# Performance work log

Hardware: AMD Instinct MI355X
Metric: run time of the kernel (lower is better)

Reference implementation:

```python
import jax, jax.numpy as jnp
import numpy as np

EMBED_DIM = 256
HEADS = 8
HEAD_DIM = EMBED_DIM // HEADS
T = 8            # time grid points
N0, N1 = 32, 32  # spatial grid
MAX_PATCH = 16   # static slot budget per cell (last slot = grid latent token)
NEG = -1e30


def construct_grid():
    g0 = jnp.linspace(0.0, 1.0, N0)
    g1 = jnp.linspace(0.0, 1.0, N1)
    G0, G1 = jnp.meshgrid(g0, g1, indexing='ij')
    return jnp.stack([G0, G1], axis=-1)  # [N0, N1, 2]


def setup_inputs() -> dict:
    key = jax.random.key(0)
    ks = jax.random.split(key, 8)
    m, n = 4, 16384
    x = jax.random.uniform(ks[0], (m, n, 3))                       # coords: (time, s0, s1) in [0,1]
    z = jax.random.normal(ks[1], (m, n, EMBED_DIM))
    time_grid = jnp.tile(jnp.linspace(0.0, 1.0, T)[None], (m, 1))  # [m, T] uniform time grid
    latents = jax.random.normal(ks[2], (N0, N1, EMBED_DIM))
    grid = construct_grid()
    s = 1.0 / np.sqrt(EMBED_DIM)
    Wq = jax.random.normal(ks[3], (EMBED_DIM, EMBED_DIM)) * s
    Wk = jax.random.normal(ks[4], (EMBED_DIM, EMBED_DIM)) * s
    Wv = jax.random.normal(ks[5], (EMBED_DIM, EMBED_DIM)) * s
    Wo = jax.random.normal(ks[6], (EMBED_DIM, EMBED_DIM)) * s
    return {'x': x, 'z': z, 'time_grid': time_grid, 'latents': latents,
            'grid': grid, 'Wq': Wq, 'Wk': Wk, 'Wv': Wv, 'Wo': Wo}


def _cumcount(idx):
    # idx: [n] int; returns per-element count of prior occurrences of the same value
    n = idx.shape[0]
    order = jnp.argsort(idx)                 # stable
    srt = idx[order]
    ar = jnp.arange(n)
    is_start = jnp.concatenate([jnp.array([True]), srt[1:] != srt[:-1]])
    seg_start = jax.lax.cummax(jnp.where(is_start, ar, 0), axis=0)
    cc = ar - seg_start
    return jnp.zeros_like(idx).at[order].set(cc.astype(idx.dtype))


def _forward(x, z, time_grid, latents, grid, Wq, Wk, Wv, Wo):
    m, n, _ = x.shape
    t = time_grid.shape[1]
    S = t * N0 * N1
    # --- build x_grid: repeat spatial grid over (m,t), insert time coord at dim 0 ---
    xg_sp = jnp.broadcast_to(grid[None, None], (m, t, N0, N1, 2))
    tg = jnp.broadcast_to(time_grid[:, :, None, None, None], (m, t, N0, N1, 1))
    x_grid = jnp.concatenate([tg, xg_sp], axis=-1)          # [m,t,N0,N1,3]
    # --- nearest gridded neighbour (k=1): per-dim rounding on the regular grid ---
    grid_shape = jnp.array([t, N0, N1], jnp.float32)
    xg_flat = x_grid.reshape(m, S, 3)
    xmin = xg_flat.min(axis=1)                               # [m,3]
    xmax = xg_flat.max(axis=1)
    spacing = (xmax - xmin) / (grid_shape - 1.0)             # [m,3]
    multi = jnp.floor((x - xmin[:, None] + spacing[:, None] / 2) / spacing[:, None])
    multi = jnp.clip(multi, 0.0, grid_shape - 1.0)
    strides = jnp.array([N0 * N1, N1, 1], jnp.float32)
    nearest = jnp.sum(multi * strides, axis=-1).astype(jnp.int32)  # [m,n] flat cell id
    # --- per-cell slot allocation via cumulative count ---
    cum = jax.vmap(_cumcount)(nearest)                       # [m,n]
    P = MAX_PATCH
    valid = cum < (P - 1)                                    # last slot reserved for grid token
    bidx = jnp.arange(m)[:, None]
    cell = jnp.where(valid, nearest, S)                      # out-of-bounds -> dropped
    slot = jnp.minimum(cum, P - 2)
    # --- scatter points into the joint grid [m, S, P, E]; slot P-1 = grid latent ---
    joint = jnp.zeros((m, S, P, EMBED_DIM), z.dtype)
    joint = joint.at[bidx, cell, slot].set(z, mode='drop')
    z_grid_flat = jnp.broadcast_to(
        latents.reshape(1, 1, N0 * N1, EMBED_DIM), (m, t, N0 * N1, EMBED_DIM)
    ).reshape(m, S, EMBED_DIM)
    joint = joint.at[:, :, P - 1].set(z_grid_flat)
    counts = jnp.zeros((m, S), jnp.int32).at[bidx, cell].add(1, mode='drop')
    counts = jnp.minimum(counts, P - 1)
    att_mask = jnp.concatenate(
        [jnp.arange(P - 1)[None, None] < counts[..., None],
         jnp.ones((m, S, 1), bool)], axis=-1)                # [m,S,P]
    # --- masked multi-head cross attention: 1 query (grid latent) per cell ---
    q = (z_grid_flat @ Wq).reshape(m, S, HEADS, HEAD_DIM)
    k = (joint @ Wk).reshape(m, S, P, HEADS, HEAD_DIM)
    v = (joint @ Wv).reshape(m, S, P, HEADS, HEAD_DIM)
    logits = jnp.einsum('mshd,msphd->mshp', q, k) / np.sqrt(HEAD_DIM)
    logits = jnp.where(att_mask[:, :, None, :], logits, NEG)
    attn = jax.nn.softmax(logits, axis=-1)
    out = jnp.einsum('mshp,msphd->mshd', attn, v).reshape(m, S, EMBED_DIM) @ Wo
    z_grid = out.reshape(m, t, N0, N1, EMBED_DIM)
    return x_grid, z_grid


def reference(x, z, time_grid, latents, grid, Wq, Wk, Wv, Wo):
    return _forward(x, z, time_grid, latents, grid, Wq, Wk, Wv, Wo)
```

## Files before the change

kernel.cpp:

```cpp
#include <hip/hip_runtime.h>
#include <hip/hip_bf16.h>

#define T_ 8
#define N0_ 32
#define N1_ 32
#define SP_ (N0_*N1_)
#define S_ (T_*SP_)
#define E_ 256
#define P_ 16
#define NH_ 8
#define HD_ 32
#define ZB_ 2048

typedef __attribute__((ext_vector_type(8))) short short8;
typedef __attribute__((ext_vector_type(4))) float f32x4;
typedef __attribute__((ext_vector_type(8))) unsigned short u16x8;

__device__ __forceinline__ unsigned short f2bf(float f) {
  __hip_bfloat16 h = __float2bfloat16(f);
  return *reinterpret_cast<unsigned short*>(&h);
}
__device__ __forceinline__ float bf2f(unsigned short u) {
  return __uint_as_float((unsigned)u << 16);
}

__device__ __forceinline__ void gl_lds16(const unsigned short* g, unsigned short* l) {
  __builtin_amdgcn_global_load_lds(
      (const __attribute__((address_space(1))) unsigned int*)(g),
      (__attribute__((address_space(3))) unsigned int*)(l), 16, 0, 0);
}

__global__ __launch_bounds__(256) void mega_prep(const float* __restrict__ z,
                                                 unsigned short* __restrict__ z16,
                                                 const float* __restrict__ Wq,
                                                 const float* __restrict__ Wk,
                                                 const float* __restrict__ Wv,
                                                 const float* __restrict__ Wo,
                                                 unsigned short* __restrict__ wT,
                                                 const float* __restrict__ latents,
                                                 unsigned short* __restrict__ lat16,
                                                 int* __restrict__ counts,
                                                 int zn8, int MS) {
  __shared__ float ts[64][65];
  int bid = blockIdx.x;
  int t = threadIdx.x;
  if (bid < ZB_) {
    int stride = ZB_ * 256;
    for (int i = bid * 256 + t; i < zn8; i += stride) {
      float4 a = *(const float4*)(z + (size_t)i * 8);
      float4 b = *(const float4*)(z + (size_t)i * 8 + 4);
      u16x8 o;
      o[0]=f2bf(a.x); o[1]=f2bf(a.y); o[2]=f2bf(a.z); o[3]=f2bf(a.w);
      o[4]=f2bf(b.x); o[5]=f2bf(b.y); o[6]=f2bf(b.z); o[7]=f2bf(b.w);
      *(u16x8*)(z16 + (size_t)i * 8) = o;
    }
  } else if (bid < ZB_ + 64) {
    int wb = bid - ZB_;
    int mat = wb >> 4;
    int tile = wb & 15;
    int tr = (tile >> 2) * 64;
    int tc = (tile & 3) * 64;
    const float* W = mat == 0 ? Wq : mat == 1 ? Wk : mat == 2 ? Wv : Wo;
    int r = t >> 2, c0 = (t & 3) * 16;
#pragma unroll
    for (int i = 0; i < 4; ++i) {
      float4 v = *(const float4*)&W[(size_t)(tr + r) * 256 + tc + c0 + i*4];
      ts[r][c0 + i*4 + 0] = v.x; ts[r][c0 + i*4 + 1] = v.y;
      ts[r][c0 + i*4 + 2] = v.z; ts[r][c0 + i*4 + 3] = v.w;
    }
    __syncthreads();
    u16x8 o0, o1;
#pragma unroll
    for (int i = 0; i < 8; ++i) o0[i] = f2bf(ts[c0 + i][r]);
#pragma unroll
    for (int i = 0; i < 8; ++i) o1[i] = f2bf(ts[c0 + 8 + i][r]);
    unsigned short* dst = wT + (size_t)(mat * 256 + tc + r) * 256 + tr + c0;
    *(u16x8*)dst = o0;
    *(u16x8*)(dst + 8) = o1;
  } else if (bid < ZB_ + 80) {
    int i0 = (bid - ZB_ - 64) * 256 + t;
    for (int i = i0; i < SP_ * E_ / 8; i += 16 * 256) {
      float4 a = *(const float4*)(latents + (size_t)i * 8);
      float4 b = *(const float4*)(latents + (size_t)i * 8 + 4);
      u16x8 o;
      o[0]=f2bf(a.x); o[1]=f2bf(a.y); o[2]=f2bf(a.z); o[3]=f2bf(a.w);
      o[4]=f2bf(b.x); o[5]=f2bf(b.y); o[6]=f2bf(b.z); o[7]=f2bf(b.w);
      *(u16x8*)(lat16 + (size_t)i * 8) = o;
    }
  } else {
    int i0 = (bid - ZB_ - 80) * 256 + t;
    for (int i = i0; i < MS / 4; i += 16 * 256)
      *(int4*)(counts + i * 4) = make_int4(0, 0, 0, 0);
  }
}

__global__ __launch_bounds__(256) void assign2_kernel(const float* __restrict__ x,
                                                      const float* __restrict__ tg,
                                                      const float* __restrict__ grid,
                                                      float* __restrict__ out,
                                                      int* __restrict__ counts,
                                                      int* __restrict__ cell_raw,
                                                      int m, int n, int tot_xg) {
  __shared__ float st[4][6];
  int tid = threadIdx.x;
  if (tid < 64) {
    float mn0 = 1e30f, mx0 = -1e30f, mn1 = 1e30f, mx1 = -1e30f;
    for (int i = tid; i < SP_; i += 64) {
      float g0 = grid[i*2], g1 = grid[i*2+1];
      mn0 = fminf(mn0, g0); mx0 = fmaxf(mx0, g0);
      mn1 = fminf(mn1, g1); mx1 = fmaxf(mx1, g1);
    }
    for (int msk = 32; msk; msk >>= 1) {
      mn0 = fminf(mn0, __shfl_xor(mn0, msk));
      mx0 = fmaxf(mx0, __shfl_xor(mx0, msk));
      mn1 = fminf(mn1, __shfl_xor(mn1, msk));
      mx1 = fmaxf(mx1, __shfl_xor(mx1, msk));
    }
    if (tid == 0) {
      for (int b = 0; b < m; ++b) {
        float tmn = 1e30f, tmx = -1e30f;
        for (int tt = 0; tt < T_; ++tt) {
          float v = tg[b*T_ + tt];
          tmn = fminf(tmn, v); tmx = fmaxf(tmx, v);
        }
        st[b][0] = tmn; st[b][1] = mn0; st[b][2] = mn1;
        st[b][3] = (tmx - tmn) / (float)(T_ - 1);
        st[b][4] = (mx0 - mn0) / (float)(N0_ - 1);
        st[b][5] = (mx1 - mn1) / (float)(N1_ - 1);
      }
    }
  }
  __syncthreads();
  int idx = blockIdx.x * 256 + tid;
  if (idx < tot_xg) {
    int sp = idx & (SP_ - 1);
    int bt = idx >> 10;
    out[idx*3 + 0] = tg[bt];
    out[idx*3 + 1] = grid[sp*2 + 0];
    out[idx*3 + 2] = grid[sp*2 + 1];
  }
  if (idx < m*n) {
    int b = idx / n;
    int j = idx - b*n;
    const float* s = st[b];
    float xt = x[(size_t)idx*3 + 0], x0 = x[(size_t)idx*3 + 1], x1 = x[(size_t)idx*3 + 2];
    float m0 = floorf((xt - s[0] + s[3]*0.5f) / s[3]);
    float m1 = floorf((x0 - s[1] + s[4]*0.5f) / s[4]);
    float m2 = floorf((x1 - s[2] + s[5]*0.5f) / s[5]);
    m0 = fminf(fmaxf(m0, 0.f), (float)(T_ - 1));
    m1 = fminf(fmaxf(m1, 0.f), (float)(N0_ - 1));
    m2 = fminf(fmaxf(m2, 0.f), (float)(N1_ - 1));
    int sc = (int)m0 * SP_ + (int)m1 * N1_ + (int)m2;
    int cg = b * S_ + sc;
    int old = atomicAdd(&counts[cg], 1);
    if (old < P_) cell_raw[(size_t)cg * P_ + old] = j;
  }
}

__global__ void finalize_kernel(const int* __restrict__ counts, int* __restrict__ cell_raw,
                                int* __restrict__ pts2, int total) {
  int cg = blockIdx.x * blockDim.x + threadIdx.x;
  if (cg >= total) return;
  int cnt = counts[cg];
  int stored = cnt < P_ ? cnt : P_;
  int eff = cnt < (P_ - 1) ? cnt : (P_ - 1);
  int* p = cell_raw + (size_t)cg * P_;
  for (int i = 1; i < stored; ++i) {
    int key = p[i]; int j = i - 1;
    while (j >= 0 && p[j] > key) { p[j+1] = p[j]; --j; }
    p[j+1] = key;
  }
  int* o = pts2 + (size_t)cg * P_;
  o[0] = eff;
  for (int i = 0; i < eff; ++i) o[1 + i] = p[i];
}

template <typename OutT>
__global__ __launch_bounds__(512, 4) void gemm_g2l(const unsigned short* __restrict__ A,
                                                   const unsigned short* __restrict__ BT,
                                                   OutT* __restrict__ C,
                                                   int M, int CP, int ldc) {
  __shared__ unsigned short lds[4][128 * 64];
  int tid = threadIdx.x;
  int nb = gridDim.x, bid = blockIdx.x;
  int L = bid;
  if ((nb & 7) == 0) L = (bid & 7) * (nb >> 3) + (bid >> 3);
  int rp = L / CP, cp = L - rp * CP;

  int wid = tid >> 6, lane = tid & 63, l15 = lane & 15, slot = lane >> 4;
  int wr = (wid >> 2) * 64, wc = (wid & 3) * 32;

  int r8 = lane >> 3, k8 = lane & 7;
  int colsw = (k8 ^ r8) << 3;
  const unsigned short* ga0 = A  + (size_t)(rp * 128 + wid * 16 + r8) * 256 + colsw;
  const unsigned short* gb0 = BT + (size_t)(cp * 128 + wid * 16 + r8) * 256 + colsw;

#define STAGE(b, kt) do { \
    const unsigned short* ga = ga0 + (kt) * 64; \
    const unsigned short* gb = gb0 + (kt) * 64; \
    gl_lds16(ga,           &lds[(b)*2    ][(wid*16    ) * 64]); \
    gl_lds16(ga + 8*256,   &lds[(b)*2    ][(wid*16 + 8) * 64]); \
    gl_lds16(gb,           &lds[(b)*2 + 1][(wid*16    ) * 64]); \
    gl_lds16(gb + 8*256,   &lds[(b)*2 + 1][(wid*16 + 8) * 64]); \
  } while (0)

  f32x4 acc[4][2] = {};
  STAGE(0, 0);

#pragma unroll
  for (int kt = 0; kt < 4; ++kt) {
    int b = kt & 1;
    if (kt < 3) STAGE(b ^ 1, kt + 1);
    if (kt < 3) asm volatile("s_waitcnt vmcnt(4)" ::: "memory");
    else        asm volatile("s_waitcnt vmcnt(0)" ::: "memory");
    __builtin_amdgcn_s_barrier();
    asm volatile("" ::: "memory");
    const unsigned short* As = lds[b*2];
    const unsigned short* Bs = lds[b*2 + 1];
#pragma unroll
    for (int kf = 0; kf < 2; ++kf) {
      short8 afr[4], bfr[2];
      int kg = kf * 4 + slot;
      int sx = kg ^ (l15 & 7);
#pragma unroll
      for (int mm = 0; mm < 4; ++mm) {
        int row = wr + mm * 16 + l15;
        afr[mm] = *(const short8*)&As[row * 64 + (sx << 3)];
      }
#pragma unroll
      for (int nn = 0; nn < 2; ++nn) {
        int col = wc + nn * 16 + l15;
        bfr[nn] = *(const short8*)&Bs[col * 64 + (sx << 3)];
      }
#pragma unroll
      for (int mm = 0; mm < 4; ++mm)
#pragma unroll
        for (int nn = 0; nn < 2; ++nn)
          acc[mm][nn] = __builtin_amdgcn_mfma_f32_16x16x32_bf16(afr[mm], bfr[nn], acc[mm][nn], 0, 0, 0);
    }
    asm volatile("" ::: "memory");
    __builtin_amdgcn_s_barrier();
    asm volatile("" ::: "memory");
  }
#undef STAGE

#pragma unroll
  for (int mm = 0; mm < 4; ++mm) {
#pragma unroll
    for (int nn = 0; nn < 2; ++nn) {
      int grow0 = rp * 128 + wr + mm * 16 + slot * 4;
      int gcol  = cp * 128 + wc + nn * 16 + l15;
#pragma unroll
      for (int j = 0; j < 4; ++j) {
        size_t o = (size_t)(grow0 + j) * ldc + gcol;
        if constexpr (__is_same(OutT, float)) C[o] = acc[mm][nn][j];
        else                                  C[o] = __float2bfloat16(acc[mm][nn][j]);
      }
    }
  }
}

__global__ __launch_bounds__(256) void attn_kernel(
    const float* __restrict__ lat,
    const __hip_bfloat16* __restrict__ kv,
    const int* __restrict__ pts2,
    __hip_bfloat16* __restrict__ attn_out, int n) {
  const float scale = 0.17677669529663687f;
  int wid = threadIdx.x >> 6;
  int lane = threadIdx.x & 63;
  int cellg = blockIdx.x * 4 + wid;
  int b = cellg >> 13;
  int c = cellg & (SP_ - 1);
  int d0 = lane << 2;

  const int* pp = pts2 + (size_t)cellg * P_;
  int4 h0 = *(const int4*)pp;
  int eff = h0.x;

  const float* latc = lat + c * 768 + d0;
  float4 q  = *(const float4*)latc;
  float4 kl = *(const float4*)(latc + 256);
  float4 vl = *(const float4*)(latc + 512);

  float part = q.x*kl.x + q.y*kl.y + q.z*kl.z + q.w*kl.w;
  part += __shfl_xor(part, 1);
  part += __shfl_xor(part, 2);
  part += __shfl_xor(part, 4);
  float mx = part * scale;
  float ssum = 1.f;
  float4 acc = vl;

  const unsigned short* kvp = (const unsigned short*)kv;
  size_t bbase = (size_t)b * n;

  int pt[4]; pt[0] = h0.y; pt[1] = h0.z; pt[2] = h0.w; pt[3] = 0;
  int done = 0, cap = 3;
  while (done < eff) {
    int np = eff - done; if (np > cap) np = cap;
    ushort4 kr[4], vr[4];
#pragma unroll
    for (int i = 0; i < 4; ++i) if (i < np) {
      size_t row = (bbase + (size_t)pt[i]) * 512;
      kr[i] = *(const ushort4*)(kvp + row + d0);
      vr[i] = *(const ushort4*)(kvp + row + 256 + d0);
    }
#pragma unroll
    for (int i = 0; i < 4; ++i) if (i < np) {
      float p = q.x*bf2f(kr[i].x) + q.y*bf2f(kr[i].y) + q.z*bf2f(kr[i].z) + q.w*bf2f(kr[i].w);
      p += __shfl_xor(p, 1);
      p += __shfl_xor(p, 2);
      p += __shfl_xor(p, 4);
      p *= scale;
      float m2 = fmaxf(mx, p);
      float corr = __expf(mx - m2);
      float e = __expf(p - m2);
      ssum = ssum * corr + e;
      acc.x = acc.x * corr + e * bf2f(vr[i].x);
      acc.y = acc.y * corr + e * bf2f(vr[i].y);
      acc.z = acc.z * corr + e * bf2f(vr[i].z);
      acc.w = acc.w * corr + e * bf2f(vr[i].w);
      mx = m2;
    }
    done += np;
    cap = 4;
    if (done < eff) {
      int4 h = *(const int4*)(pp + 1 + done);
      pt[0] = h.x; pt[1] = h.y; pt[2] = h.z; pt[3] = h.w;
    }
  }
  float inv = 1.f / ssum;
  ushort4 o;
  o.x = f2bf(acc.x * inv); o.y = f2bf(acc.y * inv);
  o.z = f2bf(acc.z * inv); o.w = f2bf(acc.w * inv);
  *(ushort4*)((unsigned short*)attn_out + (size_t)cellg * E_ + d0) = o;
}

extern "C" void kernel_launch(void* const* d_in, const int* in_sizes, int n_in,
                              void* d_out, int out_size, void* d_ws, size_t ws_size,
                              hipStream_t stream) {
  const float* x       = (const float*)d_in[0];
  const float* z       = (const float*)d_in[1];
  const float* tg      = (const float*)d_in[2];
  const float* latents = (const float*)d_in[3];
  const float* grid    = (const float*)d_in[4];
  const float* Wq      = (const float*)d_in[5];
  const float* Wk      = (const float*)d_in[6];
  const float* Wv      = (const float*)d_in[7];
  const float* Wo      = (const float*)d_in[8];

  int m = in_sizes[2] / T_;
  int n = in_sizes[1] / (m * E_);
  int MS = m * S_;
  float* out = (float*)d_out;
  int tot_xg = m * T_ * SP_;

  char* w = (char*)d_ws;
  auto alloc = [&](size_t bytes) { char* p = w; w += (bytes + 255) & ~(size_t)255; return p; };
  int*   counts     = (int*)  alloc((size_t)MS * 4);
  int*   cell_raw   = (int*)  alloc((size_t)MS * P_ * 4);
  int*   pts2       = (int*)  alloc((size_t)MS * P_ * 4);
  unsigned short* wT    = (unsigned short*)alloc((size_t)1024 * 256 * 2);
  unsigned short* lat16 = (unsigned short*)alloc((size_t)SP_ * E_ * 2);
  float* lat        = (float*)alloc((size_t)SP_ * 768 * 4);
  __hip_bfloat16* kv       = (__hip_bfloat16*)alloc((size_t)m * n * 512 * 2);
  __hip_bfloat16* attn_out = (__hip_bfloat16*)alloc((size_t)MS * E_ * 2);

  unsigned short* z16 = (unsigned short*)(out + (size_t)tot_xg * 3);

  mega_prep<<<ZB_ + 96, 256, 0, stream>>>(z, z16, Wq, Wk, Wv, Wo, wT, latents, lat16,
                                          counts, m * n * E_ / 8, MS);

  assign2_kernel<<<(m*n + 255)/256, 256, 0, stream>>>(x, tg, grid, out, counts, cell_raw,
                                                      m, n, tot_xg);

  finalize_kernel<<<(MS + 255)/256, 256, 0, stream>>>(counts, cell_raw, pts2, MS);

  gemm_g2l<float><<<48, 512, 0, stream>>>(lat16, wT, lat, SP_, 6, 768);

  gemm_g2l<__hip_bfloat16><<<2048, 512, 0, stream>>>(
      z16, wT + (size_t)256*256, (__hip_bfloat16*)kv, m*n, 4, 512);

  attn_kernel<<<MS/4, 256, 0, stream>>>(lat, kv, pts2, attn_out, n);

  gemm_g2l<float><<<512, 512, 0, stream>>>(
      (const unsigned short*)attn_out, wT + (size_t)768*256, out + (size_t)tot_xg * 3, MS, 2, 256);
}
```

Measured before the change: 104.2 us.

## Fuse fp32-to-bf16 conversion into GEMM A-loads and merge small prep kernels

Drops the separate pass that converted z and latents from fp32 to bf16. The GEMMs now stream fp32 A tiles into LDS with a swizzled layout and convert them to bf16 in registers just before the MFMAs. The weight transpose is folded into the assignment kernel, the latent GEMM shares a launch with the per-cell sort and finalize, and the counts buffer is zeroed with a memset. The goal is to cut the extra write and re-read of the bf16 copy of z, plus launch overhead. The cost is double the LDS footprint for A tiles, extra conversion work inside the GEMM inner loop, and a different launch-bounds and occupancy setting.

```diff
diff --git a/kernel.cpp b/kernel.cpp
--- a/kernel.cpp
+++ b/kernel.cpp
@@ -10,7 +10,6 @@
 #define P_ 16
 #define NH_ 8
 #define HD_ 32
-#define ZB_ 2048
 
 typedef __attribute__((ext_vector_type(8))) short short8;
 typedef __attribute__((ext_vector_type(4))) float f32x4;
@@ -24,44 +23,35 @@
   return __uint_as_float((unsigned)u << 16);
 }
 
-__device__ __forceinline__ void gl_lds16(const unsigned short* g, unsigned short* l) {
+__device__ __forceinline__ void gl_lds16(const void* g, void* l) {
   __builtin_amdgcn_global_load_lds(
       (const __attribute__((address_space(1))) unsigned int*)(g),
       (__attribute__((address_space(3))) unsigned int*)(l), 16, 0, 0);
 }
 
-__global__ __launch_bounds__(256) void mega_prep(const float* __restrict__ z,
-                                                 unsigned short* __restrict__ z16,
-                                                 const float* __restrict__ Wq,
-                                                 const float* __restrict__ Wk,
-                                                 const float* __restrict__ Wv,
-                                                 const float* __restrict__ Wo,
-                                                 unsigned short* __restrict__ wT,
-                                                 const float* __restrict__ latents,
-                                                 unsigned short* __restrict__ lat16,
-                                                 int* __restrict__ counts,
-                                                 int zn8, int MS) {
+__global__ __launch_bounds__(256) void prep_assign(const float* __restrict__ x,
+                                                   const float* __restrict__ tg,
+                                                   const float* __restrict__ grid,
+                                                   float* __restrict__ out,
+                                                   int* __restrict__ counts,
+                                                   int* __restrict__ cell_raw,
+                                                   const float* __restrict__ Wq,
+                                                   const float* __restrict__ Wk,
+                                                   const float* __restrict__ Wv,
+                                                   const float* __restrict__ Wo,
+                                                   unsigned short* __restrict__ wT,
+                                                   int m, int n, int tot_xg) {
   __shared__ float ts[64][65];
   int bid = blockIdx.x;
-  int t = threadIdx.x;
-  if (bid < ZB_) {
-    int stride = ZB_ * 256;
-    for (int i = bid * 256 + t; i < zn8; i += stride) {
-      float4 a = *(const float4*)(z + (size_t)i * 8);
-      float4 b = *(const float4*)(z + (size_t)i * 8 + 4);
-      u16x8 o;
-      o[0]=f2bf(a.x); o[1]=f2bf(a.y); o[2]=f2bf(a.z); o[3]=f2bf(a.w);
-      o[4]=f2bf(b.x); o[5]=f2bf(b.y); o[6]=f2bf(b.z); o[7]=f2bf(b.w);
-      *(u16x8*)(z16 + (size_t)i * 8) = o;
-    }
-  } else if (bid < ZB_ + 64) {
-    int wb = bid - ZB_;
+  int tid = threadIdx.x;
+  if (bid >= 256) {
+    int wb = bid - 256;
     int mat = wb >> 4;
     int tile = wb & 15;
     int tr = (tile >> 2) * 64;
     int tc = (tile & 3) * 64;
     const float* W = mat == 0 ? Wq : mat == 1 ? Wk : mat == 2 ? Wv : Wo;
-    int r = t >> 2, c0 = (t & 3) * 16;
+    int r = tid >> 2, c0 = (tid & 3) * 16;
 #pragma unroll
     for (int i = 0; i < 4; ++i) {
       float4 v = *(const float4*)&W[(size_t)(tr + r) * 256 + tc + c0 + i*4];
@@ -77,32 +67,9 @@
     unsigned short* dst = wT + (size_t)(mat * 256 + tc + r) * 256 + tr + c0;
     *(u16x8*)dst = o0;
     *(u16x8*)(dst + 8) = o1;
-  } else if (bid < ZB_ + 80) {
-    int i0 = (bid - ZB_ - 64) * 256 + t;
-    for (int i = i0; i < SP_ * E_ / 8; i += 16 * 256) {
-      float4 a = *(const float4*)(latents + (size_t)i * 8);
-      float4 b = *(const float4*)(latents + (size_t)i * 8 + 4);
-      u16x8 o;
-      o[0]=f2bf(a.x); o[1]=f2bf(a.y); o[2]=f2bf(a.z); o[3]=f2bf(a.w);
-      o[4]=f2bf(b.x); o[5]=f2bf(b.y); o[6]=f2bf(b.z); o[7]=f2bf(b.w);
-      *(u16x8*)(lat16 + (size_t)i * 8) = o;
-    }
-  } else {
-    int i0 = (bid - ZB_ - 80) * 256 + t;
-    for (int i = i0; i < MS / 4; i += 16 * 256)
-      *(int4*)(counts + i * 4) = make_int4(0, 0, 0, 0);
-  }
-}
-
-__global__ __launch_bounds__(256) void assign2_kernel(const float* __restrict__ x,
-                                                      const float* __restrict__ tg,
-                                                      const float* __restrict__ grid,
-                                                      float* __restrict__ out,
-                                                      int* __restrict__ counts,
-                                                      int* __restrict__ cell_raw,
-                                                      int m, int n, int tot_xg) {
+    return;
+  }
   __shared__ float st[4][6];
-  int tid = threadIdx.x;
   if (tid < 64) {
     float mn0 = 1e30f, mx0 = -1e30f, mn1 = 1e30f, mx1 = -1e30f;
     for (int i = tid; i < SP_; i += 64) {
@@ -131,7 +98,7 @@
     }
   }
   __syncthreads();
-  int idx = blockIdx.x * 256 + tid;
+  int idx = bid * 256 + tid;
   if (idx < tot_xg) {
     int sp = idx & (SP_ - 1);
     int bt = idx >> 10;
@@ -157,9 +124,107 @@
   }
 }
 
-__global__ void finalize_kernel(const int* __restrict__ counts, int* __restrict__ cell_raw,
-                                int* __restrict__ pts2, int total) {
-  int cg = blockIdx.x * blockDim.x + threadIdx.x;
+template <typename OutT>
+__device__ __forceinline__ void gemm_f32a_body(const float* __restrict__ A,
+                                               const unsigned short* __restrict__ BT,
+                                               OutT* __restrict__ C,
+                                               int CP, int ldc, int L, int tid) {
+  __shared__ float Af[2][128 * 32];
+  __shared__ unsigned short Bf[2][128 * 32];
+  int rp = L / CP, cp = L - rp * CP;
+
+  int wid = tid >> 6, lane = tid & 63, l15 = lane & 15, slot = lane >> 4;
+  int wr = (wid >> 2) * 64, wc = (wid & 3) * 32;
+
+  int ar = lane >> 3, ag = lane & 7;
+  const float* aSrc0 = A + (size_t)(rp * 128 + wid * 16 + ar) * 256 + ((ag ^ ar) << 2);
+  const float* aSrc1 = aSrc0 + 8 * 256;
+  int br = lane >> 2, bg = lane & 3;
+  const unsigned short* bSrc = BT + (size_t)(cp * 128 + wid * 16 + br) * 256 + ((bg ^ (br & 3)) << 3);
+
+#define STAGEF(b, kt) do { \
+    gl_lds16(aSrc0 + (kt) * 32, &Af[b][(wid * 16    ) * 32]); \
+    gl_lds16(aSrc1 + (kt) * 32, &Af[b][(wid * 16 + 8) * 32]); \
+    gl_lds16(bSrc  + (kt) * 32, &Bf[b][(wid * 16    ) * 32]); \
+  } while (0)
+
+  f32x4 acc[4][2] = {};
+  STAGEF(0, 0);
+
+#pragma unroll
+  for (int kt = 0; kt < 8; ++kt) {
+    int b = kt & 1;
+    if (kt < 7) STAGEF(b ^ 1, kt + 1);
+    if (kt < 7) asm volatile("s_waitcnt vmcnt(3)" ::: "memory");
+    else        asm volatile("s_waitcnt vmcnt(0)" ::: "memory");
+    __builtin_amdgcn_s_barrier();
+    asm volatile("" ::: "memory");
+    short8 afr[4], bfr[2];
+#pragma unroll
+    for (int mm = 0; mm < 4; ++mm) {
+      int row = wr + mm * 16 + l15;
+      int q0 = (2 * slot) ^ (row & 7);
+      int q1 = (2 * slot + 1) ^ (row & 7);
+      f32x4 a0 = *(const f32x4*)&Af[b][row * 32 + q0 * 4];
+      f32x4 a1 = *(const f32x4*)&Af[b][row * 32 + q1 * 4];
+      short8 af;
+      af[0]=f2bf(a0[0]); af[1]=f2bf(a0[1]); af[2]=f2bf(a0[2]); af[3]=f2bf(a0[3]);
+      af[4]=f2bf(a1[0]); af[5]=f2bf(a1[1]); af[6]=f2bf(a1[2]); af[7]=f2bf(a1[3]);
+      afr[mm] = af;
+    }
+#pragma unroll
+    for (int nn = 0; nn < 2; ++nn) {
+      int col = wc + nn * 16 + l15;
+      int q = slot ^ (col & 3);
+      bfr[nn] = *(const short8*)&Bf[b][col * 32 + q * 8];
+    }
+#pragma unroll
+    for (int mm = 0; mm < 4; ++mm)
+#pragma unroll
+      for (int nn = 0; nn < 2; ++nn)
+        acc[mm][nn] = __builtin_amdgcn_mfma_f32_16x16x32_bf16(afr[mm], bfr[nn], acc[mm][nn], 0, 0, 0);
+    asm volatile("" ::: "memory");
+    __builtin_amdgcn_s_barrier();
+    asm volatile("" ::: "memory");
+  }
+#undef STAGEF
+
+#pragma unroll
+  for (int mm = 0; mm < 4; ++mm) {
+#pragma unroll
+    for (int nn = 0; nn < 2; ++nn) {
+      int grow0 = rp * 128 + wr + mm * 16 + slot * 4;
+      int gcol  = cp * 128 + wc + nn * 16 + l15;
+#pragma unroll
+      for (int j = 0; j < 4; ++j) {
+        size_t o = (size_t)(grow0 + j) * ldc + gcol;
+        if constexpr (__is_same(OutT, float)) C[o] = acc[mm][nn][j];
+        else                                  C[o] = __float2bfloat16(acc[mm][nn][j]);
+      }
+    }
+  }
+}
+
+__global__ __launch_bounds__(512) void gemm_kv(const float* __restrict__ z,
+                                               const unsigned short* __restrict__ BT,
+                                               __hip_bfloat16* __restrict__ kv) {
+  int nb = gridDim.x, bid = blockIdx.x;
+  int L = (bid & 7) * (nb >> 3) + (bid >> 3);
+  gemm_f32a_body<__hip_bfloat16>(z, BT, kv, 4, 512, L, threadIdx.x);
+}
+
+__global__ __launch_bounds__(512) void phase3(const float* __restrict__ latents,
+                                              const unsigned short* __restrict__ wT,
+                                              float* __restrict__ lat,
+                                              const int* __restrict__ counts,
+                                              int* __restrict__ cell_raw,
+                                              int* __restrict__ pts2, int total) {
+  int bid = blockIdx.x;
+  if (bid < 48) {
+    gemm_f32a_body<float>(latents, wT, lat, 6, 768, bid, threadIdx.x);
+    return;
+  }
+  int cg = (bid - 48) * 512 + threadIdx.x;
   if (cg >= total) return;
   int cnt = counts[cg];
   int stored = cnt < P_ ? cnt : P_;
@@ -359,26 +424,19 @@
   int*   counts     = (int*)  alloc((size_t)MS * 4);
   int*   cell_raw   = (int*)  alloc((size_t)MS * P_ * 4);
   int*   pts2       = (int*)  alloc((size_t)MS * P_ * 4);
-  unsigned short* wT    = (unsigned short*)alloc((size_t)1024 * 256 * 2);
-  unsigned short* lat16 = (unsigned short*)alloc((size_t)SP_ * E_ * 2);
+  unsigned short* wT = (unsigned short*)alloc((size_t)1024 * 256 * 2);
   float* lat        = (float*)alloc((size_t)SP_ * 768 * 4);
   __hip_bfloat16* kv       = (__hip_bfloat16*)alloc((size_t)m * n * 512 * 2);
   __hip_bfloat16* attn_out = (__hip_bfloat16*)alloc((size_t)MS * E_ * 2);
 
-  unsigned short* z16 = (unsigned short*)(out + (size_t)tot_xg * 3);
-
-  mega_prep<<<ZB_ + 96, 256, 0, stream>>>(z, z16, Wq, Wk, Wv, Wo, wT, latents, lat16,
-                                          counts, m * n * E_ / 8, MS);
-
-  assign2_kernel<<<(m*n + 255)/256, 256, 0, stream>>>(x, tg, grid, out, counts, cell_raw,
-                                                      m, n, tot_xg);
-
-  finalize_kernel<<<(MS + 255)/256, 256, 0, stream>>>(counts, cell_raw, pts2, MS);
-
-  gemm_g2l<float><<<48, 512, 0, stream>>>(lat16, wT, lat, SP_, 6, 768);
-
-  gemm_g2l<__hip_bfloat16><<<2048, 512, 0, stream>>>(
-      z16, wT + (size_t)256*256, (__hip_bfloat16*)kv, m*n, 4, 512);
+  (void)hipMemsetAsync(counts, 0, (size_t)MS * 4, stream);
+
+  prep_assign<<<320, 256, 0, stream>>>(x, tg, grid, out, counts, cell_raw,
+                                       Wq, Wk, Wv, Wo, wT, m, n, tot_xg);
+
+  phase3<<<112, 512, 0, stream>>>(latents, wT, lat, counts, cell_raw, pts2, MS);
+
+  gemm_kv<<<2048, 512, 0, stream>>>(z, wT + (size_t)256*256, kv);
 
   attn_kernel<<<MS/4, 256, 0, stream>>>(lat, kv, pts2, attn_out, n);
 
```

After: 100.8 us. -3.2%, faster.

## Merge prep, assign, finalize and projection GEMMs into fewer launches

Applied to the files above, without the earlier changes.

Folds point-to-cell assignment into the z/weight/latent conversion kernel, and combines the KV projection GEMM, latent QKV GEMM and per-cell finalize into one heterogeneous launch. Counts zeroing moves to a hipMemsetAsync so that assignment can run in the same kernel as the conversions. The goal is fewer kernel launches and less idle tail time between small dependent stages. The risk is that blocks with different roles share one launch configuration: the 512-thread launch bounds and the GEMM's LDS footprint now also apply to the finalize blocks.

```diff
diff --git a/kernel.cpp b/kernel.cpp
--- a/kernel.cpp
+++ b/kernel.cpp
@@ -10,7 +10,6 @@
 #define P_ 16
 #define NH_ 8
 #define HD_ 32
-#define ZB_ 2048
 
 typedef __attribute__((ext_vector_type(8))) short short8;
 typedef __attribute__((ext_vector_type(4))) float f32x4;
@@ -24,29 +23,34 @@
   return __uint_as_float((unsigned)u << 16);
 }
 
-__device__ __forceinline__ void gl_lds16(const unsigned short* g, unsigned short* l) {
+__device__ __forceinline__ void gl_lds16(const void* g, void* l) {
   __builtin_amdgcn_global_load_lds(
       (const __attribute__((address_space(1))) unsigned int*)(g),
       (__attribute__((address_space(3))) unsigned int*)(l), 16, 0, 0);
 }
 
-__global__ __launch_bounds__(256) void mega_prep(const float* __restrict__ z,
-                                                 unsigned short* __restrict__ z16,
-                                                 const float* __restrict__ Wq,
-                                                 const float* __restrict__ Wk,
-                                                 const float* __restrict__ Wv,
-                                                 const float* __restrict__ Wo,
-                                                 unsigned short* __restrict__ wT,
-                                                 const float* __restrict__ latents,
-                                                 unsigned short* __restrict__ lat16,
-                                                 int* __restrict__ counts,
-                                                 int zn8, int MS) {
+__global__ __launch_bounds__(256) void prep(const float* __restrict__ z,
+                                            unsigned short* __restrict__ z16,
+                                            const float* __restrict__ x,
+                                            const float* __restrict__ tg,
+                                            const float* __restrict__ grid,
+                                            float* __restrict__ out,
+                                            int* __restrict__ counts,
+                                            int* __restrict__ cell_raw,
+                                            const float* __restrict__ Wq,
+                                            const float* __restrict__ Wk,
+                                            const float* __restrict__ Wv,
+                                            const float* __restrict__ Wo,
+                                            unsigned short* __restrict__ wT,
+                                            const float* __restrict__ latents,
+                                            unsigned short* __restrict__ lat16,
+                                            int m, int n, int tot_xg, int zn8) {
   __shared__ float ts[64][65];
+  __shared__ float st[4][6];
   int bid = blockIdx.x;
-  int t = threadIdx.x;
-  if (bid < ZB_) {
-    int stride = ZB_ * 256;
-    for (int i = bid * 256 + t; i < zn8; i += stride) {
+  int tid = threadIdx.x;
+  if (bid < 2048) {
+    for (int i = bid * 256 + tid; i < zn8; i += 2048 * 256) {
       float4 a = *(const float4*)(z + (size_t)i * 8);
       float4 b = *(const float4*)(z + (size_t)i * 8 + 4);
       u16x8 o;
@@ -54,14 +58,71 @@
       o[4]=f2bf(b.x); o[5]=f2bf(b.y); o[6]=f2bf(b.z); o[7]=f2bf(b.w);
       *(u16x8*)(z16 + (size_t)i * 8) = o;
     }
-  } else if (bid < ZB_ + 64) {
-    int wb = bid - ZB_;
+    return;
+  }
+  if (bid < 2304) {
+    if (tid < 64) {
+      float mn0 = 1e30f, mx0 = -1e30f, mn1 = 1e30f, mx1 = -1e30f;
+      for (int i = tid; i < SP_; i += 64) {
+        float g0 = grid[i*2], g1 = grid[i*2+1];
+        mn0 = fminf(mn0, g0); mx0 = fmaxf(mx0, g0);
+        mn1 = fminf(mn1, g1); mx1 = fmaxf(mx1, g1);
+      }
+      for (int msk = 32; msk; msk >>= 1) {
+        mn0 = fminf(mn0, __shfl_xor(mn0, msk));
+        mx0 = fmaxf(mx0, __shfl_xor(mx0, msk));
+        mn1 = fminf(mn1, __shfl_xor(mn1, msk));
+        mx1 = fmaxf(mx1, __shfl_xor(mx1, msk));
+      }
+      if (tid == 0) {
+        for (int b = 0; b < m; ++b) {
+          float tmn = 1e30f, tmx = -1e30f;
+          for (int tt = 0; tt < T_; ++tt) {
+            float v = tg[b*T_ + tt];
+            tmn = fminf(tmn, v); tmx = fmaxf(tmx, v);
+          }
+          st[b][0] = tmn; st[b][1] = mn0; st[b][2] = mn1;
+          st[b][3] = (tmx - tmn) / (float)(T_ - 1);
+          st[b][4] = (mx0 - mn0) / (float)(N0_ - 1);
+          st[b][5] = (mx1 - mn1) / (float)(N1_ - 1);
+        }
+      }
+    }
+    __syncthreads();
+    int idx = (bid - 2048) * 256 + tid;
+    if (idx < tot_xg) {
+      int sp = idx & (SP_ - 1);
+      int bt = idx >> 10;
+      out[idx*3 + 0] = tg[bt];
+      out[idx*3 + 1] = grid[sp*2 + 0];
+      out[idx*3 + 2] = grid[sp*2 + 1];
+    }
+    if (idx < m*n) {
+      int b = idx / n;
+      int j = idx - b*n;
+      const float* s = st[b];
+      float xt = x[(size_t)idx*3 + 0], x0 = x[(size_t)idx*3 + 1], x1 = x[(size_t)idx*3 + 2];
+      float m0 = floorf((xt - s[0] + s[3]*0.5f) / s[3]);
+      float m1 = floorf((x0 - s[1] + s[4]*0.5f) / s[4]);
+      float m2 = floorf((x1 - s[2] + s[5]*0.5f) / s[5]);
+      m0 = fminf(fmaxf(m0, 0.f), (float)(T_ - 1));
+      m1 = fminf(fmaxf(m1, 0.f), (float)(N0_ - 1));
+      m2 = fminf(fmaxf(m2, 0.f), (float)(N1_ - 1));
+      int sc = (int)m0 * SP_ + (int)m1 * N1_ + (int)m2;
+      int cg = b * S_ + sc;
+      int old = atomicAdd(&counts[cg], 1);
+      if (old < P_) cell_raw[(size_t)cg * P_ + old] = j;
+    }
+    return;
+  }
+  if (bid < 2368) {
+    int wb = bid - 2304;
     int mat = wb >> 4;
     int tile = wb & 15;
     int tr = (tile >> 2) * 64;
     int tc = (tile & 3) * 64;
     const float* W = mat == 0 ? Wq : mat == 1 ? Wk : mat == 2 ? Wv : Wo;
-    int r = t >> 2, c0 = (t & 3) * 16;
+    int r = tid >> 2, c0 = (tid & 3) * 16;
 #pragma unroll
     for (int i = 0; i < 4; ++i) {
       float4 v = *(const float4*)&W[(size_t)(tr + r) * 256 + tc + c0 + i*4];
@@ -77,89 +138,118 @@
     unsigned short* dst = wT + (size_t)(mat * 256 + tc + r) * 256 + tr + c0;
     *(u16x8*)dst = o0;
     *(u16x8*)(dst + 8) = o1;
-  } else if (bid < ZB_ + 80) {
-    int i0 = (bid - ZB_ - 64) * 256 + t;
-    for (int i = i0; i < SP_ * E_ / 8; i += 16 * 256) {
-      float4 a = *(const float4*)(latents + (size_t)i * 8);
-      float4 b = *(const float4*)(latents + (size_t)i * 8 + 4);
-      u16x8 o;
-      o[0]=f2bf(a.x); o[1]=f2bf(a.y); o[2]=f2bf(a.z); o[3]=f2bf(a.w);
-      o[4]=f2bf(b.x); o[5]=f2bf(b.y); o[6]=f2bf(b.z); o[7]=f2bf(b.w);
-      *(u16x8*)(lat16 + (size_t)i * 8) = o;
-    }
-  } else {
-    int i0 = (bid - ZB_ - 80) * 256 + t;
-    for (int i = i0; i < MS / 4; i += 16 * 256)
-      *(int4*)(counts + i * 4) = make_int4(0, 0, 0, 0);
-  }
-}
-
-__global__ __launch_bounds__(256) void assign2_kernel(const float* __restrict__ x,
-                                                      const float* __restrict__ tg,
-                                                      const float* __restrict__ grid,
-                                                      float* __restrict__ out,
-                                                      int* __restrict__ counts,
-                                                      int* __restrict__ cell_raw,
-                                                      int m, int n, int tot_xg) {
-  __shared__ float st[4][6];
-  int tid = threadIdx.x;
-  if (tid < 64) {
-    float mn0 = 1e30f, mx0 = -1e30f, mn1 = 1e30f, mx1 = -1e30f;
-    for (int i = tid; i < SP_; i += 64) {
-      float g0 = grid[i*2], g1 = grid[i*2+1];
-      mn0 = fminf(mn0, g0); mx0 = fmaxf(mx0, g0);
-      mn1 = fminf(mn1, g1); mx1 = fmaxf(mx1, g1);
-    }
-    for (int msk = 32; msk; msk >>= 1) {
-      mn0 = fminf(mn0, __shfl_xor(mn0, msk));
-      mx0 = fmaxf(mx0, __shfl_xor(mx0, msk));
-      mn1 = fminf(mn1, __shfl_xor(mn1, msk));
-      mx1 = fmaxf(mx1, __shfl_xor(mx1, msk));
-    }
-    if (tid == 0) {
-      for (int b = 0; b < m; ++b) {
-        float tmn = 1e30f, tmx = -1e30f;
-        for (int tt = 0; tt < T_; ++tt) {
-          float v = tg[b*T_ + tt];
-          tmn = fminf(tmn, v); tmx = fmaxf(tmx, v);
-        }
-        st[b][0] = tmn; st[b][1] = mn0; st[b][2] = mn1;
-        st[b][3] = (tmx - tmn) / (float)(T_ - 1);
-        st[b][4] = (mx0 - mn0) / (float)(N0_ - 1);
-        st[b][5] = (mx1 - mn1) / (float)(N1_ - 1);
-      }
-    }
-  }
-  __syncthreads();
-  int idx = blockIdx.x * 256 + tid;
-  if (idx < tot_xg) {
-    int sp = idx & (SP_ - 1);
-    int bt = idx >> 10;
-    out[idx*3 + 0] = tg[bt];
-    out[idx*3 + 1] = grid[sp*2 + 0];
-    out[idx*3 + 2] = grid[sp*2 + 1];
-  }
-  if (idx < m*n) {
-    int b = idx / n;
-    int j = idx - b*n;
-    const float* s = st[b];
-    float xt = x[(size_t)idx*3 + 0], x0 = x[(size_t)idx*3 + 1], x1 = x[(size_t)idx*3 + 2];
-    float m0 = floorf((xt - s[0] + s[3]*0.5f) / s[3]);
-    float m1 = floorf((x0 - s[1] + s[4]*0.5f) / s[4]);
-    float m2 = floorf((x1 - s[2] + s[5]*0.5f) / s[5]);
-    m0 = fminf(fmaxf(m0, 0.f), (float)(T_ - 1));
-    m1 = fminf(fmaxf(m1, 0.f), (float)(N0_ - 1));
-    m2 = fminf(fmaxf(m2, 0.f), (float)(N1_ - 1));
-    int sc = (int)m0 * SP_ + (int)m1 * N1_ + (int)m2;
-    int cg = b * S_ + sc;
-    int old = atomicAdd(&counts[cg], 1);
-    if (old < P_) cell_raw[(size_t)cg * P_ + old] = j;
-  }
-}
-
-__global__ void finalize_kernel(const int* __restrict__ counts, int* __restrict__ cell_raw,
-                                int* __restrict__ pts2, int total) {
-  int cg = blockIdx.x * blockDim.x + threadIdx.x;
+    return;
+  }
+  for (int i = (bid - 2368) * 256 + tid; i < SP_ * E_ / 8; i += 16 * 256) {
+    float4 a = *(const float4*)(latents + (size_t)i * 8);
+    float4 b = *(const float4*)(latents + (size_t)i * 8 + 4);
+    u16x8 o;
+    o[0]=f2bf(a.x); o[1]=f2bf(a.y); o[2]=f2bf(a.z); o[3]=f2bf(a.w);
+    o[4]=f2bf(b.x); o[5]=f2bf(b.y); o[6]=f2bf(b.z); o[7]=f2bf(b.w);
+    *(u16x8*)(lat16 + (size_t)i * 8) = o;
+  }
+}
+
+template <typename OutT>
+__device__ __forceinline__ void g2l_body(const unsigned short* __restrict__ A,
+                                         const unsigned short* __restrict__ BT,
+                                         OutT* __restrict__ C,
+                                         int CP, int ldc, int L, int tid) {
+  __shared__ unsigned short lds[4][128 * 64];
+  int rp = L / CP, cp = L - rp * CP;
+
+  int wid = tid >> 6, lane = tid & 63, l15 = lane & 15, slot = lane >> 4;
+  int wr = (wid >> 2) * 64, wc = (wid & 3) * 32;
+
+  int r8 = lane >> 3, k8 = lane & 7;
+  int colsw = (k8 ^ r8) << 3;
+  const unsigned short* ga0 = A  + (size_t)(rp * 128 + wid * 16 + r8) * 256 + colsw;
+  const unsigned short* gb0 = BT + (size_t)(cp * 128 + wid * 16 + r8) * 256 + colsw;
+
+#define STAGE(b, kt) do { \
+    const unsigned short* ga = ga0 + (kt) * 64; \
+    const unsigned short* gb = gb0 + (kt) * 64; \
+    gl_lds16(ga,           &lds[(b)*2    ][(wid*16    ) * 64]); \
+    gl_lds16(ga + 8*256,   &lds[(b)*2    ][(wid*16 + 8) * 64]); \
+    gl_lds16(gb,           &lds[(b)*2 + 1][(wid*16    ) * 64]); \
+    gl_lds16(gb + 8*256,   &lds[(b)*2 + 1][(wid*16 + 8) * 64]); \
+  } while (0)
+
+  f32x4 acc[4][2] = {};
+  STAGE(0, 0);
+
+#pragma unroll
+  for (int kt = 0; kt < 4; ++kt) {
+    int b = kt & 1;
+    if (kt < 3) STAGE(b ^ 1, kt + 1);
+    if (kt < 3) asm volatile("s_waitcnt vmcnt(4)" ::: "memory");
+    else        asm volatile("s_waitcnt vmcnt(0)" ::: "memory");
+    __builtin_amdgcn_s_barrier();
+    asm volatile("" ::: "memory");
+    const unsigned short* As = lds[b*2];
+    const unsigned short* Bs = lds[b*2 + 1];
+#pragma unroll
+    for (int kf = 0; kf < 2; ++kf) {
+      short8 afr[4], bfr[2];
+      int kg = kf * 4 + slot;
+      int sx = kg ^ (l15 & 7);
+#pragma unroll
+      for (int mm = 0; mm < 4; ++mm) {
+        int row = wr + mm * 16 + l15;
+        afr[mm] = *(const short8*)&As[row * 64 + (sx << 3)];
+      }
+#pragma unroll
+      for (int nn = 0; nn < 2; ++nn) {
+        int col = wc + nn * 16 + l15;
+        bfr[nn] = *(const short8*)&Bs[col * 64 + (sx << 3)];
+      }
+#pragma unroll
+      for (int mm = 0; mm < 4; ++mm)
+#pragma unroll
+        for (int nn = 0; nn < 2; ++nn)
+          acc[mm][nn] = __builtin_amdgcn_mfma_f32_16x16x32_bf16(afr[mm], bfr[nn], acc[mm][nn], 0, 0, 0);
+    }
+    asm volatile("" ::: "memory");
+    __builtin_amdgcn_s_barrier();
+    asm volatile("" ::: "memory");
+  }
+#undef STAGE
+
+#pragma unroll
+  for (int mm = 0; mm < 4; ++mm) {
+#pragma unroll
+    for (int nn = 0; nn < 2; ++nn) {
+      int grow0 = rp * 128 + wr + mm * 16 + slot * 4;
+      int gcol  = cp * 128 + wc + nn * 16 + l15;
+#pragma unroll
+      for (int j = 0; j < 4; ++j) {
+        size_t o = (size_t)(grow0 + j) * ldc + gcol;
+        if constexpr (__is_same(OutT, float)) C[o] = acc[mm][nn][j];
+        else                                  C[o] = __float2bfloat16(acc[mm][nn][j]);
+      }
+    }
+  }
+}
+
+__global__ __launch_bounds__(512, 4) void phase2(const unsigned short* __restrict__ z16,
+                                                 const unsigned short* __restrict__ wT,
+                                                 __hip_bfloat16* __restrict__ kv,
+                                                 const unsigned short* __restrict__ lat16,
+                                                 float* __restrict__ lat,
+                                                 const int* __restrict__ counts,
+                                                 int* __restrict__ cell_raw,
+                                                 int* __restrict__ pts2, int total) {
+  int bid = blockIdx.x;
+  if (bid < 2048) {
+    int L = (bid & 7) * 256 + (bid >> 3);
+    g2l_body<__hip_bfloat16>(z16, wT + (size_t)256*256, kv, 4, 512, L, threadIdx.x);
+    return;
+  }
+  if (bid < 2096) {
+    g2l_body<float>(lat16, wT, lat, 6, 768, bid - 2048, threadIdx.x);
+    return;
+  }
+  int cg = (bid - 2096) * 512 + threadIdx.x;
   if (cg >= total) return;
   int cnt = counts[cg];
   int stored = cnt < P_ ? cnt : P_;
@@ -179,85 +269,11 @@
 __global__ __launch_bounds__(512, 4) void gemm_g2l(const unsigned short* __restrict__ A,
                                                    const unsigned short* __restrict__ BT,
                                                    OutT* __restrict__ C,
-                                                   int M, int CP, int ldc) {
-  __shared__ unsigned short lds[4][128 * 64];
-  int tid = threadIdx.x;
+                                                   int CP, int ldc) {
   int nb = gridDim.x, bid = blockIdx.x;
   int L = bid;
   if ((nb & 7) == 0) L = (bid & 7) * (nb >> 3) + (bid >> 3);
-  int rp = L / CP, cp = L - rp * CP;
-
-  int wid = tid >> 6, lane = tid & 63, l15 = lane & 15, slot = lane >> 4;
-  int wr = (wid >> 2) * 64, wc = (wid & 3) * 32;
-
-  int r8 = lane >> 3, k8 = lane & 7;
-  int colsw = (k8 ^ r8) << 3;
-  const unsigned short* ga0 = A  + (size_t)(rp * 128 + wid * 16 + r8) * 256 + colsw;
-  const unsigned short* gb0 = BT + (size_t)(cp * 128 + wid * 16 + r8) * 256 + colsw;
-
-#define STAGE(b, kt) do { \
-    const unsigned short* ga = ga0 + (kt) * 64; \
-    const unsigned short* gb = gb0 + (kt) * 64; \
-    gl_lds16(ga,           &lds[(b)*2    ][(wid*16    ) * 64]); \
-    gl_lds16(ga + 8*256,   &lds[(b)*2    ][(wid*16 + 8) * 64]); \
-    gl_lds16(gb,           &lds[(b)*2 + 1][(wid*16    ) * 64]); \
-    gl_lds16(gb + 8*256,   &lds[(b)*2 + 1][(wid*16 + 8) * 64]); \
-  } while (0)
-
-  f32x4 acc[4][2] = {};
-  STAGE(0, 0);
-
-#pragma unroll
-  for (int kt = 0; kt < 4; ++kt) {
-    int b = kt & 1;
-    if (kt < 3) STAGE(b ^ 1, kt + 1);
-    if (kt < 3) asm volatile("s_waitcnt vmcnt(4)" ::: "memory");
-    else        asm volatile("s_waitcnt vmcnt(0)" ::: "memory");
-    __builtin_amdgcn_s_barrier();
-    asm volatile("" ::: "memory");
-    const unsigned short* As = lds[b*2];
-    const unsigned short* Bs = lds[b*2 + 1];
-#pragma unroll
-    for (int kf = 0; kf < 2; ++kf) {
-      short8 afr[4], bfr[2];
-      int kg = kf * 4 + slot;
-      int sx = kg ^ (l15 & 7);
-#pragma unroll
-      for (int mm = 0; mm < 4; ++mm) {
-        int row = wr + mm * 16 + l15;
-        afr[mm] = *(const short8*)&As[row * 64 + (sx << 3)];
-      }
-#pragma unroll
-      for (int nn = 0; nn < 2; ++nn) {
-        int col = wc + nn * 16 + l15;
-        bfr[nn] = *(const short8*)&Bs[col * 64 + (sx << 3)];
-      }
-#pragma unroll
-      for (int mm = 0; mm < 4; ++mm)
-#pragma unroll
-        for (int nn = 0; nn < 2; ++nn)
-          acc[mm][nn] = __builtin_amdgcn_mfma_f32_16x16x32_bf16(afr[mm], bfr[nn], acc[mm][nn], 0, 0, 0);
-    }
-    asm volatile("" ::: "memory");
-    __builtin_amdgcn_s_barrier();
-    asm volatile("" ::: "memory");
-  }
-#undef STAGE
-
-#pragma unroll
-  for (int mm = 0; mm < 4; ++mm) {
-#pragma unroll
-    for (int nn = 0; nn < 2; ++nn) {
-      int grow0 = rp * 128 + wr + mm * 16 + slot * 4;
-      int gcol  = cp * 128 + wc + nn * 16 + l15;
-#pragma unroll
-      for (int j = 0; j < 4; ++j) {
-        size_t o = (size_t)(grow0 + j) * ldc + gcol;
-        if constexpr (__is_same(OutT, float)) C[o] = acc[mm][nn][j];
-        else                                  C[o] = __float2bfloat16(acc[mm][nn][j]);
-      }
-    }
-  }
+  g2l_body<OutT>(A, BT, C, CP, ldc, L, threadIdx.x);
 }
 
 __global__ __launch_bounds__(256) void attn_kernel(
@@ -367,21 +383,16 @@
 
   unsigned short* z16 = (unsigned short*)(out + (size_t)tot_xg * 3);
 
-  mega_prep<<<ZB_ + 96, 256, 0, stream>>>(z, z16, Wq, Wk, Wv, Wo, wT, latents, lat16,
-                                          counts, m * n * E_ / 8, MS);
-
-  assign2_kernel<<<(m*n + 255)/256, 256, 0, stream>>>(x, tg, grid, out, counts, cell_raw,
-                                                      m, n, tot_xg);
-
-  finalize_kernel<<<(MS + 255)/256, 256, 0, stream>>>(counts, cell_raw, pts2, MS);
-
-  gemm_g2l<float><<<48, 512, 0, stream>>>(lat16, wT, lat, SP_, 6, 768);
-
-  gemm_g2l<__hip_bfloat16><<<2048, 512, 0, stream>>>(
-      z16, wT + (size_t)256*256, (__hip_bfloat16*)kv, m*n, 4, 512);
+  (void)hipMemsetAsync(counts, 0, (size_t)MS * 4, stream);
+
+  prep<<<2384, 256, 0, stream>>>(z, z16, x, tg, grid, out, counts, cell_raw,
+                                 Wq, Wk, Wv, Wo, wT, latents, lat16,
+                                 m, n, tot_xg, m * n * E_ / 8);
+
+  phase2<<<2160, 512, 0, stream>>>(z16, wT, kv, lat16, lat, counts, cell_raw, pts2, MS);
 
   attn_kernel<<<MS/4, 256, 0, stream>>>(lat, kv, pts2, attn_out, n);
 
   gemm_g2l<float><<<512, 512, 0, stream>>>(
-      (const unsigned short*)attn_out, wT + (size_t)768*256, out + (size_t)tot_xg * 3, MS, 2, 256);
-}
+      (const unsigned short*)attn_out, wT + (size_t)768*256, out + (size_t)tot_xg * 3, 2, 256);
+}
```

After: 112.2 us. +7.7%, slower.
